# Optimization experiments

Hardware: AMD Instinct MI355X
Metric: run time of the kernel (lower is better)

Reference implementation:

```python
import jax, jax.numpy as jnp
import numpy as np

N, C, T, V = 16, 256, 400, 27
S, CI, O = 2, 64, 256      # num_subset, inter_channels, out_channels
OFFSET = 2                  # LearnedPositionalEmbedding offset
EPS = 1e-5                  # BatchNorm eps (inference/eval mode)


def _bn(x, g, b, m, v):
    # BatchNorm2d in eval mode: (x - mean)/sqrt(var+eps)*gamma + beta, per-channel
    return (x - m[None, :, None, None]) / jnp.sqrt(v[None, :, None, None] + EPS) \
        * g[None, :, None, None] + b[None, :, None, None]


def setup_inputs() -> dict:
    key = jax.random.key(0)
    ks = jax.random.split(key, 24)
    u = lambda k, s: jax.random.uniform(k, s, jnp.float32, 0.5, 1.5)
    r = lambda k, s, sc: jax.random.normal(k, s, jnp.float32) * sc
    d = {}
    d['x'] = jax.random.normal(ks[0], (N, C, T, V), jnp.float32)
    # learned positional embedding table: (num_frame + offset, num_node)
    d['pe'] = r(ks[1], (400 + OFFSET, V), 0.02)
    # in_nets: 1x1 conv C -> 2*S*CI
    d['in_w'] = r(ks[2], (2 * S * CI, C), 0.02)
    d['in_b'] = jnp.zeros((2 * S * CI,), jnp.float32)
    d['alphas'] = jnp.ones((1, S, 1, 1), jnp.float32)
    d['att0'] = jnp.ones((1, S, V, V), jnp.float32) / V   # attention0s
    # out_nets: 1x1 conv S*C -> O, then BN1
    d['out_w'] = r(ks[3], (O, S * C), 0.02)
    d['out_b'] = jnp.zeros((O,), jnp.float32)
    d['bn1_g'] = u(ks[4], (O,)); d['bn1_b'] = r(ks[5], (O,), 0.1)
    d['bn1_m'] = r(ks[6], (O,), 0.1); d['bn1_v'] = u(ks[7], (O,))
    # ff_nets: 1x1 conv O -> O, then BN2
    d['ff_w'] = r(ks[8], (O, O), 0.02)
    d['ff_b'] = jnp.zeros((O,), jnp.float32)
    d['bn2_g'] = u(ks[9], (O,)); d['bn2_b'] = r(ks[10], (O,), 0.1)
    d['bn2_m'] = r(ks[11], (O,), 0.1); d['bn2_v'] = u(ks[12], (O,))
    # out_nett: (3,1) temporal conv O -> O, then BN3
    d['t_w'] = r(ks[13], (O, O, 3, 1), 0.02)
    d['t_b'] = jnp.zeros((O,), jnp.float32)
    d['bn3_g'] = u(ks[14], (O,)); d['bn3_b'] = r(ks[15], (O,), 0.1)
    d['bn3_m'] = r(ks[16], (O,), 0.1); d['bn3_v'] = u(ks[17], (O,))
    return d


def reference(x, pe, in_w, in_b, alphas, att0, out_w, out_b,
              bn1_g, bn1_b, bn1_m, bn1_v, ff_w, ff_b,
              bn2_g, bn2_b, bn2_m, bn2_v, t_w, t_b,
              bn3_g, bn3_b, bn3_m, bn3_v):
    n, c, t, v = x.shape
    # learned positional embedding over frame index (shared across batch*channel)
    pos = pe[jnp.arange(t) + OFFSET]              # (T, V)
    y = x + pos[None, None, :, :]                 # (N, C, T, V)
    # in_nets 1x1 conv -> q, k
    qk = jnp.einsum('nctv,oc->notv', y, in_w) + in_b[None, :, None, None]
    qk = qk.reshape(n, 2 * S, CI, t, v)
    q, k = qk[:, :S], qk[:, S:]                   # (N, S, CI, T, V) each
    attn = jnp.einsum('nsctu,nsctv->nsuv', q, k) / (CI * t) * alphas + att0
    attn = jax.nn.softmax(attn, axis=-1)          # (N, S, V, V)  (dropout p=0)
    # re-aggregate values with original x
    y2 = jnp.einsum('nctu,nsuv->nsctv', x, attn).reshape(n, S * c, t, v)
    y2 = jnp.einsum('nctv,oc->notv', y2, out_w) + out_b[None, :, None, None]
    y2 = _bn(y2, bn1_g, bn1_b, bn1_m, bn1_v)
    y1 = jax.nn.leaky_relu(x + y2, 0.1)           # downs1 = identity (C==O)
    y2 = jnp.einsum('nctv,oc->notv', y1, ff_w) + ff_b[None, :, None, None]
    y2 = _bn(y2, bn2_g, bn2_b, bn2_m, bn2_v)
    y1 = jax.nn.leaky_relu(x + y2, 0.1)           # downs2 = identity
    # temporal branch (use_temporal_att=False): (3,1) conv + BN + residual
    z = jax.lax.conv_general_dilated(
        y1, t_w, window_strides=(1, 1), padding=((1, 1), (0, 0)),
        dimension_numbers=('NCHW', 'OIHW', 'NCHW')) + t_b[None, :, None, None]
    z = _bn(z, bn3_g, bn3_b, bn3_m, bn3_v)
    return jax.nn.leaky_relu(y1 + z, 0.1)         # downt2 = identity
```

## Files before the change

### kernel.cpp

```cpp
#include <hip/hip_runtime.h>
#include <hip/hip_bf16.h>
#include <cstddef>

#define NBATCH 16
#define CCH    256
#define TT     400
#define VV     27
#define TV     10800
#define EPSV   1e-5f
#define P2     10854

typedef __attribute__((ext_vector_type(8))) short  short8;
typedef __attribute__((ext_vector_type(4))) float  floatx4;

__device__ __forceinline__ unsigned short f2bu(float f) {
    __hip_bfloat16 h = __float2bfloat16(f);
    return *(unsigned short*)&h;
}
__device__ __forceinline__ float bu2f(unsigned short u) {
    union { float f; unsigned int i; } c; c.i = ((unsigned int)u) << 16; return c.f;
}
__device__ __forceinline__ void gl_lds16(const void* g, void* l) {
    __builtin_amdgcn_global_load_lds(
        (const __attribute__((address_space(1))) void*)g,
        (__attribute__((address_space(3))) void*)l, 16, 0, 0);
}

template<int KC, int MODE>
__global__ __launch_bounds__(256) void mfma_gemm(
    const unsigned short* __restrict__ X8,
    const unsigned short* __restrict__ W8,
    const float* __restrict__ bias,
    const float* __restrict__ bng, const float* __restrict__ bnb,
    const float* __restrict__ bnm, const float* __restrict__ bnv,
    const void* __restrict__ resv,
    float* __restrict__ outf,
    unsigned short* __restrict__ out8)
{
    constexpr int XPITCH = (MODE == 3) ? P2 : TV;
    constexpr int XOFF   = (MODE == 3) ? 27 : 0;
    constexpr int XROWS  = (MODE == 3) ? 32 : (KC / 8);
    constexpr int OPITCH = (MODE == 2) ? P2 : TV;
    constexpr int OOFF   = (MODE == 2) ? 27 : 0;

    __shared__ short Ws[4096];
    __shared__ short Xs[4096];
    __shared__ float scs[128], shs[128];

    const int tid  = threadIdx.x;
    const int wid  = tid >> 6;
    const int lane = tid & 63;
    const int quad = lane >> 4, col = lane & 15;
    const int n  = blockIdx.z;
    const int p0 = blockIdx.x * 128;
    const int o0 = blockIdx.y * 128;
    const int wo = (wid >> 1) * 64;
    const int wp = (wid & 1) * 64;

    const size_t nX = (size_t)n * XROWS * XPITCH;

    floatx4 acc[4][4];
    #pragma unroll
    for (int i = 0; i < 4; i++)
        #pragma unroll
        for (int j = 0; j < 4; j++)
            acc[i][j] = (floatx4){0.f, 0.f, 0.f, 0.f};

    for (int k0 = 0; k0 < KC; k0 += 32) {
        int c0 = k0, pshift = 0;
        if constexpr (MODE == 3) {
            int kt = k0 >> 8;
            c0 = k0 & 255;
            pshift = 27 * (kt - 1);
        }
        __syncthreads();
        #pragma unroll
        for (int q = 0; q < 2; q++) {
            const int ci = wid * 2 + q;
            const int kg = ci >> 1, half = ci & 1;
            const size_t woff = ((size_t)((k0 >> 3) + kg) * 256 + o0 + half * 64 + lane) * 8;
            gl_lds16(W8 + woff, Ws + ci * 512);
            const size_t xoff = (nX + (size_t)((c0 >> 3) + kg) * XPITCH
                                 + XOFF + p0 + pshift + half * 64 + lane) * 8;
            gl_lds16(X8 + xoff, Xs + ci * 512);
        }
        __syncthreads();
        short8 a[4], b[4];
        #pragma unroll
        for (int i = 0; i < 4; i++)
            a[i] = *(const short8*)&Ws[quad * 1024 + (wo + i * 16 + col) * 8];
        #pragma unroll
        for (int j = 0; j < 4; j++)
            b[j] = *(const short8*)&Xs[quad * 1024 + (wp + j * 16 + col) * 8];
        #pragma unroll
        for (int i = 0; i < 4; i++)
            #pragma unroll
            for (int j = 0; j < 4; j++)
                acc[i][j] = __builtin_amdgcn_mfma_f32_16x16x32_bf16(a[i], b[j], acc[i][j], 0, 0, 0);
    }

    __syncthreads();
    if (tid < 128) {
        const int o = o0 + tid;
        float sc, sh;
        if constexpr (MODE == 0) { sc = 1.f; sh = bias[o]; }
        else {
            const float g = bng[o], b2 = bnb[o], m = bnm[o], v2 = bnv[o];
            sc = g * rsqrtf(v2 + EPSV);
            sh = bias[o] * sc + b2 - m * sc;
        }
        scs[tid] = sc; shs[tid] = sh;
    }
    __syncthreads();

    const float* resf = (const float*)resv;
    const unsigned short* res8 = (const unsigned short*)resv;

    #pragma unroll
    for (int i = 0; i < 4; i++) {
        const int ol = wo + i * 16 + quad * 4;
        const int ob = o0 + ol;
        #pragma unroll
        for (int j = 0; j < 4; j++) {
            const int p = p0 + wp + j * 16 + col;
            if (p >= TV) continue;
            float v[4];
            #pragma unroll
            for (int r = 0; r < 4; r++)
                v[r] = acc[i][j][r] * scs[ol + r] + shs[ol + r];
            if constexpr (MODE == 3) {
                const size_t roff = ((size_t)n * 32 * P2 + (size_t)(ob >> 3) * P2 + 27 + p) * 8 + (ob & 7);
                union { unsigned long long u64; unsigned short us[4]; } rr;
                rr.u64 = *(const unsigned long long*)&res8[roff];
                #pragma unroll
                for (int r = 0; r < 4; r++) {
                    float t = v[r] + bu2f(rr.us[r]);
                    t = t > 0.f ? t : 0.1f * t;
                    outf[((size_t)n * 256 + ob + r) * TV + p] = t;
                }
            } else {
                union { unsigned long long u64; unsigned short us[4]; } pk;
                #pragma unroll
                for (int r = 0; r < 4; r++) {
                    float t = v[r];
                    if constexpr (MODE != 0) {
                        t += resf[((size_t)n * 256 + ob + r) * TV + p];
                        t = t > 0.f ? t : 0.1f * t;
                    }
                    pk.us[r] = f2bu(t);
                }
                *(unsigned long long*)&out8[((size_t)n * 32 * OPITCH
                    + (size_t)(ob >> 3) * OPITCH + OOFF + p) * 8 + (ob & 7)] = pk.u64;
            }
        }
    }
}

__global__ __launch_bounds__(256) void prep_xpe(
    const float* __restrict__ x, const float* __restrict__ pe,
    unsigned short* __restrict__ xpe8)
{
    const int p = blockIdx.x * 256 + threadIdx.x;
    const int cg = blockIdx.y, n = blockIdx.z;
    if (p >= TV) return;
    const float pev = pe[p + 54];
    const float* xp = x + ((size_t)n * 256 + cg * 8) * TV + p;
    union { unsigned short us[8]; uint4 q; } pk;
    #pragma unroll
    for (int r = 0; r < 8; r++)
        pk.us[r] = f2bu(xp[(size_t)r * TV] + pev);
    *(uint4*)&xpe8[(((size_t)n * 32 + cg) * TV + p) * 8] = pk.q;
}

__global__ void pack_w(const float* __restrict__ w, unsigned short* __restrict__ w8,
                       int KCc, int conv)
{
    const int idx = blockIdx.x * 256 + threadIdx.x;
    if (idx >= 256 * KCc) return;
    const int o = idx / KCc, k = idx - o * KCc;
    float v;
    if (conv) { const int c = k & 255, kt = k >> 8; v = w[((size_t)o * 256 + c) * 3 + kt]; }
    else v = w[(size_t)o * KCc + k];
    w8[((size_t)(k >> 3) * 256 + o) * 8 + (k & 7)] = f2bu(v);
}

__global__ void zero_pads(unsigned short* __restrict__ y1b8) {
    unsigned short* base = y1b8 + (size_t)blockIdx.x * P2 * 8;
    for (int i = threadIdx.x; i < 27 * 8; i += 256) {
        base[i] = 0;
        base[10827 * 8 + i] = 0;
    }
}

__global__ __launch_bounds__(256) void attn_logits_mfma(
    const unsigned short* __restrict__ qk8, float* __restrict__ logits)
{
    __shared__ float red[4][32][33];
    const int tid  = threadIdx.x;
    const int wid  = tid >> 6;
    const int lane = tid & 63;
    const int quad = lane >> 4, col = lane & 15;
    const int tch = blockIdx.x;
    const int ns  = blockIdx.y;
    const int n = ns >> 1, s = ns & 1;
    const int t0 = tch * 16 + wid * 4;

    const unsigned short* qb = qk8 + (size_t)(n * 32 + s * 8) * TV * 8;
    const unsigned short* kb = qk8 + (size_t)(n * 32 + 16 + s * 8) * TV * 8;

    floatx4 acc[2][2];
    #pragma unroll
    for (int i = 0; i < 2; i++)
        #pragma unroll
        for (int j = 0; j < 2; j++)
            acc[i][j] = (floatx4){0.f, 0.f, 0.f, 0.f};

    #pragma unroll
    for (int ti = 0; ti < 4; ti++) {
        const int t = t0 + ti;
        #pragma unroll
        for (int kk = 0; kk < 2; kk++) {
            const size_t ro = ((size_t)(kk * 4 + quad) * TV + t * 27 + col) * 8;
            const short8 a0 = *(const short8*)&qb[ro];
            const short8 a1 = *(const short8*)&qb[ro + 128];
            const short8 b0 = *(const short8*)&kb[ro];
            const short8 b1 = *(const short8*)&kb[ro + 128];
            acc[0][0] = __builtin_amdgcn_mfma_f32_16x16x32_bf16(a0, b0, acc[0][0], 0, 0, 0);
            acc[0][1] = __builtin_amdgcn_mfma_f32_16x16x32_bf16(a0, b1, acc[0][1], 0, 0, 0);
            acc[1][0] = __builtin_amdgcn_mfma_f32_16x16x32_bf16(a1, b0, acc[1][0], 0, 0, 0);
            acc[1][1] = __builtin_amdgcn_mfma_f32_16x16x32_bf16(a1, b1, acc[1][1], 0, 0, 0);
        }
    }

    #pragma unroll
    for (int i = 0; i < 2; i++)
        #pragma unroll
        for (int j = 0; j < 2; j++)
            #pragma unroll
            for (int r = 0; r < 4; r++)
                red[wid][i * 16 + quad * 4 + r][j * 16 + col] = acc[i][j][r];
    __syncthreads();
    for (int e = tid; e < 729; e += 256) {
        const int u = e / 27, v = e - u * 27;
        atomicAdd(&logits[(size_t)ns * 729 + e],
                  red[0][u][v] + red[1][u][v] + red[2][u][v] + red[3][u][v]);
    }
}

__global__ __launch_bounds__(64) void attn_softmax(
    const float* __restrict__ logits, const float* __restrict__ alphas,
    const float* __restrict__ att0, float* __restrict__ attn)
{
    const int ns = blockIdx.x;
    const int s = ns & 1;
    const int u = threadIdx.x;
    if (u < 27) {
        float row[27];
        const float alpha = alphas[s];
        const float inv_ct = 1.f / 25600.f;
        float m = -1e30f;
        for (int v = 0; v < 27; v++) {
            const float val = logits[(size_t)ns * 729 + u * 27 + v] * inv_ct * alpha
                            + att0[(size_t)(s * 27 + u) * 27 + v];
            row[v] = val;
            m = fmaxf(m, val);
        }
        float sum = 0.f;
        for (int v = 0; v < 27; v++) { row[v] = __expf(row[v] - m); sum += row[v]; }
        const float inv = 1.f / sum;
        for (int v = 0; v < 27; v++)
            attn[(size_t)ns * 729 + u * 27 + v] = row[v] * inv;
    }
}

__global__ __launch_bounds__(256) void xa_mfma(
    const float* __restrict__ x, const float* __restrict__ attn,
    unsigned short* __restrict__ xa8)
{
    __shared__ unsigned short xs[16][16][40];
    const int tid  = threadIdx.x;
    const int wid  = tid >> 6;
    const int lane = tid & 63;
    const int quad = lane >> 4, col = lane & 15;
    const int tch = blockIdx.x;
    const int c0  = blockIdx.y * 16;
    const int n   = blockIdx.z;

    short8 bf[2][2];
    #pragma unroll
    for (int s = 0; s < 2; s++) {
        const float* ab = attn + (size_t)(n * 2 + s) * 729;
        #pragma unroll
        for (int vt = 0; vt < 2; vt++) {
            const int v = vt * 16 + col;
            #pragma unroll
            for (int e = 0; e < 8; e++) {
                const int u = quad * 8 + e;
                bf[s][vt][e] = (u < 27 && v < 27) ? (short)f2bu(ab[u * 27 + v]) : (short)0;
            }
        }
    }

    for (int idx = tid; idx < 16 * 16 * 5; idx += 256) {
        const int t = idx / 80;
        const int r = idx - t * 80;
        const int c = r / 5;
        xs[t][c][27 + (r - c * 5)] = 0;
    }

    const float* xbase = x + ((size_t)n * 256 + c0) * TV + tch * 432;
    for (int idx = tid; idx < 16 * 108; idx += 256) {
        const int row = idx / 108;
        const int q   = idx - row * 108;
        const int j   = q * 4;
        int t = (j * 607) >> 14;
        int u = j - t * 27;
        const float4 f = *(const float4*)&xbase[(size_t)row * TV + j];
        float e4[4] = {f.x, f.y, f.z, f.w};
        #pragma unroll
        for (int r = 0; r < 4; r++) {
            xs[t][row][u] = f2bu(e4[r]);
            if (++u == 27) { u = 0; ++t; }
        }
    }
    __syncthreads();

    #pragma unroll
    for (int ti = 0; ti < 4; ti++) {
        const int tl = wid * 4 + ti;
        const int t  = tch * 16 + tl;
        const short8 af = *(const short8*)&xs[tl][col][quad * 8];
        #pragma unroll
        for (int s = 0; s < 2; s++) {
            #pragma unroll
            for (int vt = 0; vt < 2; vt++) {
                floatx4 d = __builtin_amdgcn_mfma_f32_16x16x32_bf16(
                    af, bf[s][vt], (floatx4){0.f, 0.f, 0.f, 0.f}, 0, 0, 0);
                const int v = vt * 16 + col;
                if (v < 27) {
                    const size_t cgg = (size_t)n * 64 + s * 32 + (c0 >> 3) + (quad >> 1);
                    union { unsigned long long u64; unsigned short us[4]; } pk;
                    #pragma unroll
                    for (int r = 0; r < 4; r++) pk.us[r] = f2bu(d[r]);
                    *(unsigned long long*)&xa8[(cgg * TV + t * 27 + v) * 8 + (quad & 1) * 4] = pk.u64;
                }
            }
        }
    }
}

extern "C" void kernel_launch(void* const* d_in, const int* in_sizes, int n_in,
                              void* d_out, int out_size, void* d_ws, size_t ws_size,
                              hipStream_t stream) {
    const float* x      = (const float*)d_in[0];
    const float* pe     = (const float*)d_in[1];
    const float* in_w   = (const float*)d_in[2];
    const float* in_b   = (const float*)d_in[3];
    const float* alphas = (const float*)d_in[4];
    const float* att0   = (const float*)d_in[5];
    const float* out_w  = (const float*)d_in[6];
    const float* out_b  = (const float*)d_in[7];
    const float* bn1_g  = (const float*)d_in[8];
    const float* bn1_b  = (const float*)d_in[9];
    const float* bn1_m  = (const float*)d_in[10];
    const float* bn1_v  = (const float*)d_in[11];
    const float* ff_w   = (const float*)d_in[12];
    const float* ff_b   = (const float*)d_in[13];
    const float* bn2_g  = (const float*)d_in[14];
    const float* bn2_b  = (const float*)d_in[15];
    const float* bn2_m  = (const float*)d_in[16];
    const float* bn2_v  = (const float*)d_in[17];
    const float* t_w    = (const float*)d_in[18];
    const float* t_b    = (const float*)d_in[19];
    const float* bn3_g  = (const float*)d_in[20];
    const float* bn3_b  = (const float*)d_in[21];
    const float* bn3_m  = (const float*)d_in[22];
    const float* bn3_v  = (const float*)d_in[23];

    char* ws = (char*)d_ws;
    const size_t A_BYTES = (size_t)16 * 32 * TV * 8 * 2 + 8192;
    const size_t B_BYTES = (size_t)16 * 256 * TV * 4 + 8192;
    const size_t C_BYTES = (size_t)16 * 32 * P2 * 8 * 2 + 8192;
    unsigned short* xpe8 = (unsigned short*)ws;
    unsigned short* y1_8 = (unsigned short*)ws;
    unsigned short* qk8  = (unsigned short*)(ws + A_BYTES);
    unsigned short* xa8  = (unsigned short*)(ws + A_BYTES);
    unsigned short* y1b8 = (unsigned short*)(ws + A_BYTES + B_BYTES);
    char* D = ws + A_BYTES + B_BYTES + C_BYTES;
    float* logits = (float*)D;
    float* attn   = (float*)(D + 93440);
    unsigned short* w1_8 = (unsigned short*)(D + 2 * 93440);
    unsigned short* w4_8 = w1_8 + (size_t)256 * 256;
    unsigned short* w5_8 = w4_8 + (size_t)256 * 512;
    unsigned short* w6_8 = w5_8 + (size_t)256 * 256;

    pack_w<<<256, 256, 0, stream>>>(in_w,  w1_8, 256, 0);
    pack_w<<<512, 256, 0, stream>>>(out_w, w4_8, 512, 0);
    pack_w<<<256, 256, 0, stream>>>(ff_w,  w5_8, 256, 0);
    pack_w<<<768, 256, 0, stream>>>(t_w,   w6_8, 768, 1);
    prep_xpe<<<dim3(43, 32, 16), 256, 0, stream>>>(x, pe, xpe8);
    zero_pads<<<512, 256, 0, stream>>>(y1b8);

    dim3 gg((TV + 127) / 128, 2, NBATCH);

    mfma_gemm<256, 0><<<gg, 256, 0, stream>>>(
        xpe8, w1_8, in_b, nullptr, nullptr, nullptr, nullptr, nullptr, nullptr, qk8);

    hipMemsetAsync(logits, 0, (size_t)NBATCH * 2 * 729 * sizeof(float), stream);
    attn_logits_mfma<<<dim3(25, NBATCH * 2), 256, 0, stream>>>(qk8, logits);
    attn_softmax<<<NBATCH * 2, 64, 0, stream>>>(logits, alphas, att0, attn);

    xa_mfma<<<dim3(25, 16, 16), 256, 0, stream>>>(x, attn, xa8);

    mfma_gemm<512, 1><<<gg, 256, 0, stream>>>(
        xa8, w4_8, out_b, bn1_g, bn1_b, bn1_m, bn1_v, x, nullptr, y1_8);

    mfma_gemm<256, 2><<<gg, 256, 0, stream>>>(
        y1_8, w5_8, ff_b, bn2_g, bn2_b, bn2_m, bn2_v, x, nullptr, y1b8);

    mfma_gemm<768, 3><<<gg, 256, 0, stream>>>(
        y1b8, w6_8, t_b, bn3_g, bn3_b, bn3_m, bn3_v, y1b8, (float*)d_out, nullptr);
}
```

Measured before the change: 839.9 us.

## Read residual from packed bf16 x+pe instead of fp32 x in GEMM epilogues

The MODE 1 and MODE 2 epilogues now take the residual from the bf16 channel-packed xpe8 buffer and subtract pe, instead of gathering fp32 x with strided per-channel loads. This halves residual traffic and makes the loads contiguous. Workspace buffers are reassigned so xpe8 stays alive, and the pad-zeroing launch moves after the first out GEMM. The temporal conv K loop is reordered to iterate the three taps per channel chunk, for better cache reuse of input rows. The residual now carries bf16 rounding error and pe cancellation, which slightly reduces accuracy.

```diff
diff --git a/kernel.cpp b/kernel.cpp
--- a/kernel.cpp
+++ b/kernel.cpp
@@ -33,7 +33,8 @@
     const float* __restrict__ bias,
     const float* __restrict__ bng, const float* __restrict__ bnb,
     const float* __restrict__ bnm, const float* __restrict__ bnv,
-    const void* __restrict__ resv,
+    const unsigned short* __restrict__ res8,
+    const float* __restrict__ pe,
     float* __restrict__ outf,
     unsigned short* __restrict__ out8)
 {
@@ -66,12 +67,17 @@
         for (int j = 0; j < 4; j++)
             acc[i][j] = (floatx4){0.f, 0.f, 0.f, 0.f};
 
-    for (int k0 = 0; k0 < KC; k0 += 32) {
-        int c0 = k0, pshift = 0;
+    for (int step = 0; step < KC / 32; ++step) {
+        int k0, c0, pshift = 0;
         if constexpr (MODE == 3) {
-            int kt = k0 >> 8;
-            c0 = k0 & 255;
+            const int ccs = step / 3;
+            const int kt  = step - ccs * 3;
+            k0 = kt * 256 + ccs * 32;
+            c0 = ccs * 32;
             pshift = 27 * (kt - 1);
+        } else {
+            k0 = step * 32;
+            c0 = k0;
         }
         __syncthreads();
         #pragma unroll
@@ -112,9 +118,6 @@
         scs[tid] = sc; shs[tid] = sh;
     }
     __syncthreads();
-
-    const float* resf = (const float*)resv;
-    const unsigned short* res8 = (const unsigned short*)resv;
 
     #pragma unroll
     for (int i = 0; i < 4; i++) {
@@ -138,15 +141,22 @@
                     t = t > 0.f ? t : 0.1f * t;
                     outf[((size_t)n * 256 + ob + r) * TV + p] = t;
                 }
+            } else if constexpr (MODE == 0) {
+                union { unsigned long long u64; unsigned short us[4]; } pk;
+                #pragma unroll
+                for (int r = 0; r < 4; r++) pk.us[r] = f2bu(v[r]);
+                *(unsigned long long*)&out8[((size_t)n * 32 * TV
+                    + (size_t)(ob >> 3) * TV + p) * 8 + (ob & 7)] = pk.u64;
             } else {
+                const float pev = pe[p + 54];
+                const size_t roff = ((size_t)n * 32 * TV + (size_t)(ob >> 3) * TV + p) * 8 + (ob & 7);
+                union { unsigned long long u64; unsigned short us[4]; } rr;
+                rr.u64 = *(const unsigned long long*)&res8[roff];
                 union { unsigned long long u64; unsigned short us[4]; } pk;
                 #pragma unroll
                 for (int r = 0; r < 4; r++) {
-                    float t = v[r];
-                    if constexpr (MODE != 0) {
-                        t += resf[((size_t)n * 256 + ob + r) * TV + p];
-                        t = t > 0.f ? t : 0.1f * t;
-                    }
+                    float t = v[r] + (bu2f(rr.us[r]) - pev);
+                    t = t > 0.f ? t : 0.1f * t;
                     pk.us[r] = f2bu(t);
                 }
                 *(unsigned long long*)&out8[((size_t)n * 32 * OPITCH
@@ -382,10 +392,10 @@
     const size_t B_BYTES = (size_t)16 * 256 * TV * 4 + 8192;
     const size_t C_BYTES = (size_t)16 * 32 * P2 * 8 * 2 + 8192;
     unsigned short* xpe8 = (unsigned short*)ws;
-    unsigned short* y1_8 = (unsigned short*)ws;
     unsigned short* qk8  = (unsigned short*)(ws + A_BYTES);
     unsigned short* xa8  = (unsigned short*)(ws + A_BYTES);
-    unsigned short* y1b8 = (unsigned short*)(ws + A_BYTES + B_BYTES);
+    unsigned short* y1b8 = (unsigned short*)(ws + A_BYTES);
+    unsigned short* y1_8 = (unsigned short*)(ws + A_BYTES + B_BYTES);
     char* D = ws + A_BYTES + B_BYTES + C_BYTES;
     float* logits = (float*)D;
     float* attn   = (float*)(D + 93440);
@@ -399,12 +409,11 @@
     pack_w<<<256, 256, 0, stream>>>(ff_w,  w5_8, 256, 0);
     pack_w<<<768, 256, 0, stream>>>(t_w,   w6_8, 768, 1);
     prep_xpe<<<dim3(43, 32, 16), 256, 0, stream>>>(x, pe, xpe8);
-    zero_pads<<<512, 256, 0, stream>>>(y1b8);
 
     dim3 gg((TV + 127) / 128, 2, NBATCH);
 
     mfma_gemm<256, 0><<<gg, 256, 0, stream>>>(
-        xpe8, w1_8, in_b, nullptr, nullptr, nullptr, nullptr, nullptr, nullptr, qk8);
+        xpe8, w1_8, in_b, nullptr, nullptr, nullptr, nullptr, nullptr, nullptr, nullptr, qk8);
 
     hipMemsetAsync(logits, 0, (size_t)NBATCH * 2 * 729 * sizeof(float), stream);
     attn_logits_mfma<<<dim3(25, NBATCH * 2), 256, 0, stream>>>(qk8, logits);
@@ -413,11 +422,13 @@
     xa_mfma<<<dim3(25, 16, 16), 256, 0, stream>>>(x, attn, xa8);
 
     mfma_gemm<512, 1><<<gg, 256, 0, stream>>>(
-        xa8, w4_8, out_b, bn1_g, bn1_b, bn1_m, bn1_v, x, nullptr, y1_8);
+        xa8, w4_8, out_b, bn1_g, bn1_b, bn1_m, bn1_v, xpe8, pe, nullptr, y1_8);
+
+    zero_pads<<<512, 256, 0, stream>>>(y1b8);
 
     mfma_gemm<256, 2><<<gg, 256, 0, stream>>>(
-        y1_8, w5_8, ff_b, bn2_g, bn2_b, bn2_m, bn2_v, x, nullptr, y1b8);
+        y1_8, w5_8, ff_b, bn2_g, bn2_b, bn2_m, bn2_v, xpe8, pe, nullptr, y1b8);
 
     mfma_gemm<768, 3><<<gg, 256, 0, stream>>>(
-        y1b8, w6_8, t_b, bn3_g, bn3_b, bn3_m, bn3_v, y1b8, (float*)d_out, nullptr);
-}
+        y1b8, w6_8, t_b, bn3_g, bn3_b, bn3_m, bn3_v, y1b8, nullptr, (float*)d_out, nullptr);
+}
```

After: 830.9 us. Within noise of the previous version (-1.1%).
